# Kernel optimization log

Measured on AMD Instinct MI355X. Metric: run time of the kernel, lower is better.

The kernel has to match this reference:

```python
import jax, jax.numpy as jnp
import numpy as np

N_NODES = 100000


def _graph_conv(h, src, dst, W_rel, W_root, b):
    # PyG GraphConv with aggr='add':
    # out = lin_rel(scatter_add(h[src] -> dst)) + lin_root(h) + bias
    agg = jax.ops.segment_sum(h[src], dst, num_segments=N_NODES)  # [N, D]
    return agg @ W_rel.T + h @ W_root.T + b


def setup_inputs() -> dict:
    key = jax.random.key(0)
    ks = jax.random.split(key, 8)
    N, D, E = N_NODES, 128, 1600000
    s = 1.0 / np.sqrt(D)
    x = jax.random.normal(ks[0], (N, D), dtype=jnp.float32)
    edge_index = jax.random.randint(ks[1], (2, E), 0, N, dtype=jnp.int64)
    W1_rel = jax.random.normal(ks[2], (D, D), dtype=jnp.float32) * s
    W1_root = jax.random.normal(ks[3], (D, D), dtype=jnp.float32) * s
    b1 = jnp.zeros((D,), dtype=jnp.float32)
    W2_rel = jax.random.normal(ks[4], (D, D), dtype=jnp.float32) * s
    W2_root = jax.random.normal(ks[5], (D, D), dtype=jnp.float32) * s
    b2 = jnp.zeros((D,), dtype=jnp.float32)
    return {"x": x, "edge_index": edge_index, "W1_rel": W1_rel,
            "W1_root": W1_root, "b1": b1, "W2_rel": W2_rel,
            "W2_root": W2_root, "b2": b2}


def reference(x, edge_index, W1_rel, W1_root, b1, W2_rel, W2_root, b2):
    src, dst = edge_index[0], edge_index[1]
    h = _graph_conv(x, src, dst, W1_rel, W1_root, b1)
    h = jax.nn.relu(h)
    out = _graph_conv(h, src, dst, W2_rel, W2_root, b2)
    return out
```

## Files before the change

kernel.cpp:

```cpp
#include <hip/hip_runtime.h>

#define NN 100000
#define DIM 128
#define NE 1600000
#define NCHUNK 64
#define FILL_CHUNK (NE / NCHUNK)

typedef __attribute__((ext_vector_type(8))) short short8;
typedef __attribute__((ext_vector_type(4))) float f32x4;

__device__ __forceinline__ unsigned f2b(float f) {
    unsigned u = __float_as_uint(f);
    return (u + 0x7FFFu + ((u >> 16) & 1u)) >> 16;
}
__device__ __forceinline__ float blo(unsigned v) { return __uint_as_float(v << 16); }
__device__ __forceinline__ float bhi(unsigned v) { return __uint_as_float(v & 0xFFFF0000u); }

__device__ __forceinline__ long long didx(long long pos, int is64) {
    return is64 ? 2 * pos : pos;
}

__global__ void detect_kernel(const void* __restrict__ ei, int* __restrict__ flag) {
    __shared__ int any;
    if (threadIdx.x == 0) any = 0;
    __syncthreads();
    const int* p = (const int*)ei;
    int nz = 0;
    for (int i = threadIdx.x; i < 2048; i += 256) nz |= (p[2 * i + 1] != 0);
    if (nz) any = 1;
    __syncthreads();
    if (threadIdx.x == 0) flag[0] = any ? 0 : 1;
}

__global__ void cvt_kernel(const float* __restrict__ in, unsigned short* __restrict__ out, int n8) {
    int i = blockIdx.x * 256 + threadIdx.x;
    if (i >= n8) return;
    const float4* p = (const float4*)in + (size_t)i * 2;
    float4 a = p[0], b = p[1];
    uint4 o;
    o.x = f2b(a.x) | (f2b(a.y) << 16);
    o.y = f2b(a.z) | (f2b(a.w) << 16);
    o.z = f2b(b.x) | (f2b(b.y) << 16);
    o.w = f2b(b.z) | (f2b(b.w) << 16);
    ((uint4*)out)[i] = o;
}

__global__ void cvtw_kernel(const float* __restrict__ w0, const float* __restrict__ w1,
                            const float* __restrict__ w2, const float* __restrict__ w3,
                            unsigned short* __restrict__ o0, unsigned short* __restrict__ o1,
                            unsigned short* __restrict__ o2, unsigned short* __restrict__ o3) {
    int i = blockIdx.x * 256 + threadIdx.x;
    int which = i >> 11, j = i & 2047;
    const float* in = which == 0 ? w0 : which == 1 ? w1 : which == 2 ? w2 : w3;
    unsigned short* out = which == 0 ? o0 : which == 1 ? o1 : which == 2 ? o2 : o3;
    const float4* p = (const float4*)in + (size_t)j * 2;
    float4 a = p[0], b = p[1];
    uint4 o;
    o.x = f2b(a.x) | (f2b(a.y) << 16);
    o.y = f2b(a.z) | (f2b(a.w) << 16);
    o.z = f2b(b.x) | (f2b(b.y) << 16);
    o.w = f2b(b.z) | (f2b(b.w) << 16);
    ((uint4*)out)[j] = o;
}

__global__ void hist_kernel(const void* __restrict__ ei, int* __restrict__ deg,
                            const int* __restrict__ flag, int E) {
    int is64 = flag[0];
    const int* p = (const int*)ei;
    int base = blockIdx.x * 1024 + threadIdx.x;
    int d0 = -1, d1 = -1, d2 = -1, d3 = -1;
    if (base + 0 * 256 < E) d0 = p[didx((long long)E + base + 0 * 256, is64)];
    if (base + 1 * 256 < E) d1 = p[didx((long long)E + base + 1 * 256, is64)];
    if (base + 2 * 256 < E) d2 = p[didx((long long)E + base + 2 * 256, is64)];
    if (base + 3 * 256 < E) d3 = p[didx((long long)E + base + 3 * 256, is64)];
    if (d0 >= 0) atomicAdd(&deg[d0], 1);
    if (d1 >= 0) atomicAdd(&deg[d1], 1);
    if (d2 >= 0) atomicAdd(&deg[d2], 1);
    if (d3 >= 0) atomicAdd(&deg[d3], 1);
}

__global__ void scan1(const int* __restrict__ deg, int* __restrict__ offsets,
                      int* __restrict__ bsum, int n) {
    __shared__ int wsum[4];
    int t = threadIdx.x, lane = t & 63, w = t >> 6;
    int base = blockIdx.x * 1024 + t * 4;
    int a0 = base + 0 < n ? deg[base + 0] : 0;
    int a1 = base + 1 < n ? deg[base + 1] : 0;
    int a2 = base + 2 < n ? deg[base + 2] : 0;
    int a3 = base + 3 < n ? deg[base + 3] : 0;
    int s = a0 + a1 + a2 + a3;
    int x = s;
#pragma unroll
    for (int off = 1; off < 64; off <<= 1) {
        int y = __shfl_up(x, off, 64);
        if (lane >= off) x += y;
    }
    if (lane == 63) wsum[w] = x;
    __syncthreads();
    if (t == 0) {
        int c = 0;
#pragma unroll
        for (int k = 0; k < 4; k++) { int tmp = wsum[k]; wsum[k] = c; c += tmp; }
        bsum[blockIdx.x] = c;
    }
    __syncthreads();
    int excl = wsum[w] + (x - s);
    if (base + 0 < n) offsets[base + 0] = excl;
    if (base + 1 < n) offsets[base + 1] = excl + a0;
    if (base + 2 < n) offsets[base + 2] = excl + a0 + a1;
    if (base + 3 < n) offsets[base + 3] = excl + a0 + a1 + a2;
}

__global__ void scan2(int* __restrict__ bsum, int* __restrict__ offsets, int nb, int n) {
    __shared__ int w0tot;
    int t = threadIdx.x, lane = t & 63, w = t >> 6;
    int v = t < nb ? bsum[t] : 0;
    int x = v;
#pragma unroll
    for (int off = 1; off < 64; off <<= 1) {
        int y = __shfl_up(x, off, 64);
        if (lane >= off) x += y;
    }
    if (t == 63) w0tot = x;
    __syncthreads();
    int excl = x - v + (w ? w0tot : 0);
    if (t < nb) bsum[t] = excl;
    if (t == nb - 1) offsets[n] = excl + v;
}

__global__ void scan3(int* __restrict__ offsets, int* __restrict__ cursor,
                      const int* __restrict__ bsum, int n) {
    int base = blockIdx.x * 1024 + threadIdx.x * 4;
    int add = bsum[blockIdx.x];
#pragma unroll
    for (int j = 0; j < 4; j++) {
        int i = base + j;
        if (i < n) { int v = offsets[i] + add; offsets[i] = v; cursor[i] = v; }
    }
}

__global__ __launch_bounds__(256)
void fill_kernel(const void* __restrict__ ei, int* __restrict__ cursor,
                 int* __restrict__ csr_src, const int* __restrict__ flag,
                 int* __restrict__ claim, int E) {
    const int c = blockIdx.x >> 3;
    const int is64 = flag[0];
    const int* p = (const int*)ei;
    const int t = threadIdx.x;

    int xcd;
    asm volatile("s_getreg_b32 %0, hwreg(HW_REG_XCC_ID)" : "=s"(xcd));
    xcd &= 7;

    __shared__ int s_r;
    if (t == 0) {
        int got = -1;
#pragma unroll
        for (int k = 0; k < 8; k++) {
            int r = (xcd + k) & 7;
            if (atomicCAS(&claim[c * 8 + r], 0, 1) == 0) { got = r; break; }
        }
        s_r = got;
    }
    __syncthreads();
    const int r = s_r;
    if (r < 0) return;

    const int lo = r * (NN / 8), hi = lo + (NN / 8);
    const int beg = c * FILL_CHUNK;
    const int end = min(beg + FILL_CHUNK, E);
    for (int i = beg + t; i < end; i += 1024) {
        int e1 = i + 256, e2 = i + 512, e3 = i + 768;
        int d0 = p[didx((long long)E + i, is64)];
        int d1 = e1 < end ? p[didx((long long)E + e1, is64)] : -1;
        int d2 = e2 < end ? p[didx((long long)E + e2, is64)] : -1;
        int d3 = e3 < end ? p[didx((long long)E + e3, is64)] : -1;
        if (d0 >= lo && d0 < hi) csr_src[atomicAdd(&cursor[d0], 1)] = p[didx(i, is64)];
        if (d1 >= lo && d1 < hi) csr_src[atomicAdd(&cursor[d1], 1)] = p[didx(e1, is64)];
        if (d2 >= lo && d2 < hi) csr_src[atomicAdd(&cursor[d2], 1)] = p[didx(e2, is64)];
        if (d3 >= lo && d3 < hi) csr_src[atomicAdd(&cursor[d3], 1)] = p[didx(e3, is64)];
    }
}

__global__ void agg_kernel(const unsigned* __restrict__ hb,
                           const int* __restrict__ offsets,
                           const int* __restrict__ csr,
                           unsigned* __restrict__ aggb, int n) {
    int node = blockIdx.x * 4 + (threadIdx.x >> 6);
    int lane = threadIdx.x & 63;
    if (node >= n) return;
    int e = offsets[node], end = offsets[node + 1];
    float lo4[4] = {0.f, 0.f, 0.f, 0.f}, hi4[4] = {0.f, 0.f, 0.f, 0.f};
    for (; e + 8 <= end; e += 8) {
        int idx[8];
        unsigned vv[8];
#pragma unroll
        for (int j = 0; j < 8; j++) idx[j] = csr[e + j];
#pragma unroll
        for (int j = 0; j < 8; j++) vv[j] = hb[idx[j] * 64 + lane];
#pragma unroll
        for (int j = 0; j < 8; j++) { lo4[j & 3] += blo(vv[j]); hi4[j & 3] += bhi(vv[j]); }
    }
    for (; e + 4 <= end; e += 4) {
        int idx[4];
        unsigned vv[4];
#pragma unroll
        for (int j = 0; j < 4; j++) idx[j] = csr[e + j];
#pragma unroll
        for (int j = 0; j < 4; j++) vv[j] = hb[idx[j] * 64 + lane];
#pragma unroll
        for (int j = 0; j < 4; j++) { lo4[j] += blo(vv[j]); hi4[j] += bhi(vv[j]); }
    }
    for (; e < end; ++e) {
        unsigned v = hb[csr[e] * 64 + lane];
        lo4[0] += blo(v); hi4[0] += bhi(v);
    }
    float s0 = (lo4[0] + lo4[1]) + (lo4[2] + lo4[3]);
    float s1 = (hi4[0] + hi4[1]) + (hi4[2] + hi4[3]);
    aggb[node * 64 + lane] = f2b(s0) | (f2b(s1) << 16);
}

template <int OUTF32>
__global__ __launch_bounds__(256, 2)
void mfma_gemm(const unsigned short* __restrict__ A,
               const unsigned short* __restrict__ H,
               const unsigned short* __restrict__ Wr,
               const unsigned short* __restrict__ Wt,
               const float* __restrict__ bias,
               void* __restrict__ outp, int n) {
    __shared__ __align__(16) char sIn[128 * 256];
    __shared__ __align__(16) char sW[128 * 256];
    int t = threadIdx.x;
    int l = t & 63, w = t >> 6;
    int row0 = blockIdx.x * 128;
    int lr = l & 15;
    int lk = (l >> 4) << 3;

    f32x4 acc[2][8];
#pragma unroll
    for (int i = 0; i < 2; i++)
#pragma unroll
        for (int j = 0; j < 8; j++) acc[i][j] = (f32x4){0.f, 0.f, 0.f, 0.f};

    for (int phase = 0; phase < 2; ++phase) {
        const unsigned short* In = phase ? H : A;
        const unsigned short* W = phase ? Wt : Wr;
        __syncthreads();
#pragma unroll
        for (int q = 0; q < 8; q++) {
            int idx = q * 256 + t;
            int r = idx >> 4, c = idx & 15;
            int gr = row0 + r; if (gr > n - 1) gr = n - 1;
            uint4 v = ((const uint4*)In)[(size_t)gr * 16 + c];
            *(uint4*)(sIn + r * 256 + ((c * 16) ^ ((r & 7) << 4))) = v;
            uint4 wv = ((const uint4*)W)[r * 16 + c];
            *(uint4*)(sW + r * 256 + ((c * 16) ^ ((r & 7) << 4))) = wv;
        }
        __syncthreads();
#pragma unroll
        for (int ks = 0; ks < 4; ++ks) {
            int kb = (ks * 32 + lk) * 2;
            short8 av[2], bv[8];
#pragma unroll
            for (int mt = 0; mt < 2; mt++) {
                int r = w * 32 + mt * 16 + lr;
                av[mt] = *(const short8*)(sIn + r * 256 + (kb ^ ((r & 7) << 4)));
            }
#pragma unroll
            for (int nt = 0; nt < 8; nt++) {
                int cw = nt * 16 + lr;
                bv[nt] = *(const short8*)(sW + cw * 256 + (kb ^ ((cw & 7) << 4)));
            }
#pragma unroll
            for (int mt = 0; mt < 2; mt++)
#pragma unroll
                for (int nt = 0; nt < 8; nt++)
                    acc[mt][nt] = __builtin_amdgcn_mfma_f32_16x16x32_bf16(
                        av[mt], bv[nt], acc[mt][nt], 0, 0, 0);
        }
    }

    int rbase = row0 + w * 32 + ((l >> 4) << 2);
#pragma unroll
    for (int mt = 0; mt < 2; mt++) {
#pragma unroll
        for (int nt = 0; nt < 8; nt++) {
            int col = nt * 16 + lr;
            float bc = bias[col];
#pragma unroll
            for (int j = 0; j < 4; j++) {
                int row = rbase + mt * 16 + j;
                if (row < n) {
                    float v = acc[mt][nt][j] + bc;
                    if (OUTF32) {
                        ((float*)outp)[(size_t)row * DIM + col] = v;
                    } else {
                        v = fmaxf(v, 0.f);
                        ((unsigned short*)outp)[(size_t)row * DIM + col] =
                            (unsigned short)f2b(v);
                    }
                }
            }
        }
    }
}

extern "C" void kernel_launch(void* const* d_in, const int* in_sizes, int n_in,
                              void* d_out, int out_size, void* d_ws, size_t ws_size,
                              hipStream_t stream) {
    const int N = NN, E = NE;
    const float* x = (const float*)d_in[0];
    const void* ei = d_in[1];
    const float* W1r = (const float*)d_in[2];
    const float* W1t = (const float*)d_in[3];
    const float* b1 = (const float*)d_in[4];
    const float* W2r = (const float*)d_in[5];
    const float* W2t = (const float*)d_in[6];
    const float* b2 = (const float*)d_in[7];
    float* out = (float*)d_out;

    char* wsp = (char*)d_ws;
    auto alloc = [&](size_t bytes) {
        char* p = wsp;
        wsp += (bytes + 255) & ~(size_t)255;
        return p;
    };
    int* flag = (int*)alloc(4);
    int* deg = (int*)alloc((size_t)N * 4);
    int* claim = (int*)alloc((size_t)NCHUNK * 8 * 4);
    int* offsets = (int*)alloc((size_t)(N + 1) * 4);
    int* cursor = (int*)alloc((size_t)N * 4);
    int* bsum = (int*)alloc(512);
    int* csr_src = (int*)alloc((size_t)E * 4);
    unsigned short* w1rb = (unsigned short*)alloc(DIM * DIM * 2);
    unsigned short* w1tb = (unsigned short*)alloc(DIM * DIM * 2);
    unsigned short* w2rb = (unsigned short*)alloc(DIM * DIM * 2);
    unsigned short* w2tb = (unsigned short*)alloc(DIM * DIM * 2);
    unsigned short* xb = (unsigned short*)alloc((size_t)N * DIM * 2);
    unsigned short* aggb = (unsigned short*)alloc((size_t)N * DIM * 2);

    const int NB = (N + 1023) / 1024;

    hipMemsetAsync(deg, 0, (size_t)N * 4, stream);
    hipMemsetAsync(claim, 0, (size_t)NCHUNK * 8 * 4, stream);
    detect_kernel<<<1, 256, 0, stream>>>(ei, flag);

    cvt_kernel<<<(N * DIM / 8 + 255) / 256, 256, 0, stream>>>(x, xb, N * DIM / 8);
    cvtw_kernel<<<32, 256, 0, stream>>>(W1r, W1t, W2r, W2t, w1rb, w1tb, w2rb, w2tb);

    hist_kernel<<<(E + 1023) / 1024, 256, 0, stream>>>(ei, deg, flag, E);
    scan1<<<NB, 256, 0, stream>>>(deg, offsets, bsum, N);
    scan2<<<1, 128, 0, stream>>>(bsum, offsets, NB, N);
    scan3<<<NB, 256, 0, stream>>>(offsets, cursor, bsum, N);
    fill_kernel<<<NCHUNK * 8, 256, 0, stream>>>(ei, cursor, csr_src, flag, claim, E);

    agg_kernel<<<N / 4, 256, 0, stream>>>((const unsigned*)xb, offsets, csr_src,
                                          (unsigned*)aggb, N);
    mfma_gemm<0><<<(N + 127) / 128, 256, 0, stream>>>(aggb, xb, w1rb, w1tb, b1, xb, N);

    agg_kernel<<<N / 4, 256, 0, stream>>>((const unsigned*)xb, offsets, csr_src,
                                          (unsigned*)aggb, N);
    mfma_gemm<1><<<(N + 127) / 128, 256, 0, stream>>>(aggb, xb, w2rb, w2tb, b2, out, N);
}
```

Before: 455.0 us.

## Build CSR via two-level binned counting sort with shared-memory atomics

Replaces the global-atomic histogram, three-pass scan and XCD-partitioned atomic fill with a two-level bucket sort. Destinations are first binned into 128-node bins using per-block shared-memory histograms and scatter cursors, with packed (local dst, src) words staged in the aggregation buffer. A per-bin kernel then counts and places edges inside each bin to produce offsets and the CSR. The aim is to remove contended global atomics and scattered global writes during CSR construction. In exchange it adds a single-block scan over 64x782 counts and an extra pass over the edges.

```diff
diff --git a/kernel.cpp b/kernel.cpp
--- a/kernel.cpp
+++ b/kernel.cpp
@@ -3,8 +3,10 @@
 #define NN 100000
 #define DIM 128
 #define NE 1600000
-#define NCHUNK 64
-#define FILL_CHUNK (NE / NCHUNK)
+#define BINW 128
+#define NBIN 782
+#define NSB 64
+#define SCHUNK (NE / NSB)
 
 typedef __attribute__((ext_vector_type(8))) short short8;
 typedef __attribute__((ext_vector_type(4))) float f32x4;
@@ -63,33 +65,38 @@
     ((uint4*)out)[j] = o;
 }
 
-__global__ void hist_kernel(const void* __restrict__ ei, int* __restrict__ deg,
-                            const int* __restrict__ flag, int E) {
-    int is64 = flag[0];
+__global__ __launch_bounds__(512)
+void binhist_kernel(const void* __restrict__ ei, const int* __restrict__ flag,
+                    int* __restrict__ bcnt) {
+    __shared__ int h[NBIN];
+    for (int k = threadIdx.x; k < NBIN; k += 512) h[k] = 0;
+    __syncthreads();
+    const int is64 = flag[0];
     const int* p = (const int*)ei;
-    int base = blockIdx.x * 1024 + threadIdx.x;
-    int d0 = -1, d1 = -1, d2 = -1, d3 = -1;
-    if (base + 0 * 256 < E) d0 = p[didx((long long)E + base + 0 * 256, is64)];
-    if (base + 1 * 256 < E) d1 = p[didx((long long)E + base + 1 * 256, is64)];
-    if (base + 2 * 256 < E) d2 = p[didx((long long)E + base + 2 * 256, is64)];
-    if (base + 3 * 256 < E) d3 = p[didx((long long)E + base + 3 * 256, is64)];
-    if (d0 >= 0) atomicAdd(&deg[d0], 1);
-    if (d1 >= 0) atomicAdd(&deg[d1], 1);
-    if (d2 >= 0) atomicAdd(&deg[d2], 1);
-    if (d3 >= 0) atomicAdd(&deg[d3], 1);
-}
-
-__global__ void scan1(const int* __restrict__ deg, int* __restrict__ offsets,
-                      int* __restrict__ bsum, int n) {
-    __shared__ int wsum[4];
+    const int beg = blockIdx.x * SCHUNK, end = beg + SCHUNK;
+    for (int i = beg + (int)threadIdx.x; i < end; i += 512) {
+        unsigned b = ((unsigned)p[didx((long long)NE + i, is64)]) >> 7;
+        if (b < NBIN) atomicAdd(&h[b], 1);
+    }
+    __syncthreads();
+    for (int k = threadIdx.x; k < NBIN; k += 512)
+        bcnt[blockIdx.x * NBIN + k] = h[k];
+}
+
+__global__ __launch_bounds__(1024)
+void binscan_kernel(const int* __restrict__ bcnt, int* __restrict__ start,
+                    int* __restrict__ binofs) {
+    __shared__ int tot[NBIN];
+    __shared__ int wsum[16];
     int t = threadIdx.x, lane = t & 63, w = t >> 6;
-    int base = blockIdx.x * 1024 + t * 4;
-    int a0 = base + 0 < n ? deg[base + 0] : 0;
-    int a1 = base + 1 < n ? deg[base + 1] : 0;
-    int a2 = base + 2 < n ? deg[base + 2] : 0;
-    int a3 = base + 3 < n ? deg[base + 3] : 0;
-    int s = a0 + a1 + a2 + a3;
-    int x = s;
+    for (int k = t; k < NBIN; k += 1024) {
+        int s = 0;
+        for (int b = 0; b < NSB; b++) s += bcnt[b * NBIN + k];
+        tot[k] = s;
+    }
+    __syncthreads();
+    int v = (t < NBIN) ? tot[t] : 0;
+    int x = v;
 #pragma unroll
     for (int off = 1; off < 64; off <<= 1) {
         int y = __shfl_up(x, off, 64);
@@ -97,88 +104,92 @@
     }
     if (lane == 63) wsum[w] = x;
     __syncthreads();
-    if (t == 0) {
-        int c = 0;
-#pragma unroll
-        for (int k = 0; k < 4; k++) { int tmp = wsum[k]; wsum[k] = c; c += tmp; }
-        bsum[blockIdx.x] = c;
-    }
-    __syncthreads();
-    int excl = wsum[w] + (x - s);
-    if (base + 0 < n) offsets[base + 0] = excl;
-    if (base + 1 < n) offsets[base + 1] = excl + a0;
-    if (base + 2 < n) offsets[base + 2] = excl + a0 + a1;
-    if (base + 3 < n) offsets[base + 3] = excl + a0 + a1 + a2;
-}
-
-__global__ void scan2(int* __restrict__ bsum, int* __restrict__ offsets, int nb, int n) {
-    __shared__ int w0tot;
-    int t = threadIdx.x, lane = t & 63, w = t >> 6;
-    int v = t < nb ? bsum[t] : 0;
-    int x = v;
-#pragma unroll
-    for (int off = 1; off < 64; off <<= 1) {
-        int y = __shfl_up(x, off, 64);
-        if (lane >= off) x += y;
-    }
-    if (t == 63) w0tot = x;
-    __syncthreads();
-    int excl = x - v + (w ? w0tot : 0);
-    if (t < nb) bsum[t] = excl;
-    if (t == nb - 1) offsets[n] = excl + v;
-}
-
-__global__ void scan3(int* __restrict__ offsets, int* __restrict__ cursor,
-                      const int* __restrict__ bsum, int n) {
-    int base = blockIdx.x * 1024 + threadIdx.x * 4;
-    int add = bsum[blockIdx.x];
-#pragma unroll
-    for (int j = 0; j < 4; j++) {
-        int i = base + j;
-        if (i < n) { int v = offsets[i] + add; offsets[i] = v; cursor[i] = v; }
-    }
-}
-
-__global__ __launch_bounds__(256)
-void fill_kernel(const void* __restrict__ ei, int* __restrict__ cursor,
-                 int* __restrict__ csr_src, const int* __restrict__ flag,
-                 int* __restrict__ claim, int E) {
-    const int c = blockIdx.x >> 3;
+    if (w == 0) {
+        int s = (lane < 16) ? wsum[lane] : 0;
+#pragma unroll
+        for (int off = 1; off < 16; off <<= 1) {
+            int y = __shfl_up(s, off, 64);
+            if (lane >= off) s += y;
+        }
+        if (lane < 16) wsum[lane] = s;
+    }
+    __syncthreads();
+    int excl = (w ? wsum[w - 1] : 0) + (x - v);
+    if (t < NBIN) binofs[t] = excl;
+    if (t == NBIN - 1) binofs[NBIN] = excl + v;
+    __syncthreads();
+    for (int k = t; k < NBIN; k += 1024) {
+        int acc = binofs[k];
+        for (int b = 0; b < NSB; b++) {
+            start[b * NBIN + k] = acc;
+            acc += bcnt[b * NBIN + k];
+        }
+    }
+}
+
+__global__ __launch_bounds__(512)
+void binscatter_kernel(const void* __restrict__ ei, const int* __restrict__ flag,
+                       const int* __restrict__ start, unsigned* __restrict__ ebin) {
+    __shared__ int cur[NBIN];
+    for (int k = threadIdx.x; k < NBIN; k += 512)
+        cur[k] = start[blockIdx.x * NBIN + k];
+    __syncthreads();
     const int is64 = flag[0];
     const int* p = (const int*)ei;
-    const int t = threadIdx.x;
-
-    int xcd;
-    asm volatile("s_getreg_b32 %0, hwreg(HW_REG_XCC_ID)" : "=s"(xcd));
-    xcd &= 7;
-
-    __shared__ int s_r;
+    const int beg = blockIdx.x * SCHUNK, end = beg + SCHUNK;
+    for (int i = beg + (int)threadIdx.x; i < end; i += 2048) {
+        int dd[4], ss[4];
+#pragma unroll
+        for (int j = 0; j < 4; j++) {
+            int e = i + j * 512;
+            if (e < end) {
+                dd[j] = p[didx((long long)NE + e, is64)];
+                ss[j] = p[didx(e, is64)];
+            } else { dd[j] = -1; ss[j] = 0; }
+        }
+#pragma unroll
+        for (int j = 0; j < 4; j++) {
+            unsigned b = ((unsigned)dd[j]) >> 7;
+            if (dd[j] >= 0 && b < NBIN) {
+                int pos = atomicAdd(&cur[b], 1);
+                if ((unsigned)pos < (unsigned)NE)
+                    ebin[pos] = ((unsigned)(dd[j] & 127) << 17) | (unsigned)ss[j];
+            }
+        }
+    }
+}
+
+__global__ __launch_bounds__(256)
+void binfin_kernel(const unsigned* __restrict__ ebin, const int* __restrict__ binofs,
+                   int* __restrict__ offsets, int* __restrict__ csr) {
+    __shared__ int cnt[BINW];
+    __shared__ int excl[BINW];
+    int t = threadIdx.x;
+    if (t < BINW) cnt[t] = 0;
+    __syncthreads();
+    int k = blockIdx.x;
+    int beg = binofs[k];
+    int end = binofs[k + 1];
+    if (beg < 0) beg = 0;
+    if (end > NE) end = NE;
+    for (int i = beg + t; i < end; i += 256) atomicAdd(&cnt[ebin[i] >> 17], 1);
+    __syncthreads();
     if (t == 0) {
-        int got = -1;
-#pragma unroll
-        for (int k = 0; k < 8; k++) {
-            int r = (xcd + k) & 7;
-            if (atomicCAS(&claim[c * 8 + r], 0, 1) == 0) { got = r; break; }
-        }
-        s_r = got;
-    }
-    __syncthreads();
-    const int r = s_r;
-    if (r < 0) return;
-
-    const int lo = r * (NN / 8), hi = lo + (NN / 8);
-    const int beg = c * FILL_CHUNK;
-    const int end = min(beg + FILL_CHUNK, E);
-    for (int i = beg + t; i < end; i += 1024) {
-        int e1 = i + 256, e2 = i + 512, e3 = i + 768;
-        int d0 = p[didx((long long)E + i, is64)];
-        int d1 = e1 < end ? p[didx((long long)E + e1, is64)] : -1;
-        int d2 = e2 < end ? p[didx((long long)E + e2, is64)] : -1;
-        int d3 = e3 < end ? p[didx((long long)E + e3, is64)] : -1;
-        if (d0 >= lo && d0 < hi) csr_src[atomicAdd(&cursor[d0], 1)] = p[didx(i, is64)];
-        if (d1 >= lo && d1 < hi) csr_src[atomicAdd(&cursor[d1], 1)] = p[didx(e1, is64)];
-        if (d2 >= lo && d2 < hi) csr_src[atomicAdd(&cursor[d2], 1)] = p[didx(e2, is64)];
-        if (d3 >= lo && d3 < hi) csr_src[atomicAdd(&cursor[d3], 1)] = p[didx(e3, is64)];
+        int a = 0;
+        for (int r = 0; r < BINW; r++) { excl[r] = a; a += cnt[r]; }
+    }
+    __syncthreads();
+    if (t < BINW) {
+        int node = k * BINW + t;
+        if (node < NN) offsets[node] = beg + excl[t];
+        cnt[t] = excl[t];
+    }
+    if (k == 0 && t == 0) offsets[NN] = NE;
+    __syncthreads();
+    for (int i = beg + t; i < end; i += 256) {
+        unsigned c = ebin[i];
+        int pos = atomicAdd(&cnt[c >> 17], 1);
+        if (beg + pos < NE) csr[beg + pos] = (int)(c & 0x1FFFF);
     }
 }
 
@@ -308,7 +319,7 @@
 extern "C" void kernel_launch(void* const* d_in, const int* in_sizes, int n_in,
                               void* d_out, int out_size, void* d_ws, size_t ws_size,
                               hipStream_t stream) {
-    const int N = NN, E = NE;
+    const int N = NN;
     const float* x = (const float*)d_in[0];
     const void* ei = d_in[1];
     const float* W1r = (const float*)d_in[2];
@@ -326,39 +337,34 @@
         return p;
     };
     int* flag = (int*)alloc(4);
-    int* deg = (int*)alloc((size_t)N * 4);
-    int* claim = (int*)alloc((size_t)NCHUNK * 8 * 4);
+    int* bcnt = (int*)alloc((size_t)NSB * NBIN * 4);
+    int* start = (int*)alloc((size_t)NSB * NBIN * 4);
+    int* binofs = (int*)alloc((size_t)(NBIN + 1) * 4);
     int* offsets = (int*)alloc((size_t)(N + 1) * 4);
-    int* cursor = (int*)alloc((size_t)N * 4);
-    int* bsum = (int*)alloc(512);
-    int* csr_src = (int*)alloc((size_t)E * 4);
+    int* csr = (int*)alloc((size_t)NE * 4);
     unsigned short* w1rb = (unsigned short*)alloc(DIM * DIM * 2);
     unsigned short* w1tb = (unsigned short*)alloc(DIM * DIM * 2);
     unsigned short* w2rb = (unsigned short*)alloc(DIM * DIM * 2);
     unsigned short* w2tb = (unsigned short*)alloc(DIM * DIM * 2);
     unsigned short* xb = (unsigned short*)alloc((size_t)N * DIM * 2);
     unsigned short* aggb = (unsigned short*)alloc((size_t)N * DIM * 2);
-
-    const int NB = (N + 1023) / 1024;
-
-    hipMemsetAsync(deg, 0, (size_t)N * 4, stream);
-    hipMemsetAsync(claim, 0, (size_t)NCHUNK * 8 * 4, stream);
+    unsigned* ebin = (unsigned*)aggb;
+
     detect_kernel<<<1, 256, 0, stream>>>(ei, flag);
 
     cvt_kernel<<<(N * DIM / 8 + 255) / 256, 256, 0, stream>>>(x, xb, N * DIM / 8);
     cvtw_kernel<<<32, 256, 0, stream>>>(W1r, W1t, W2r, W2t, w1rb, w1tb, w2rb, w2tb);
 
-    hist_kernel<<<(E + 1023) / 1024, 256, 0, stream>>>(ei, deg, flag, E);
-    scan1<<<NB, 256, 0, stream>>>(deg, offsets, bsum, N);
-    scan2<<<1, 128, 0, stream>>>(bsum, offsets, NB, N);
-    scan3<<<NB, 256, 0, stream>>>(offsets, cursor, bsum, N);
-    fill_kernel<<<NCHUNK * 8, 256, 0, stream>>>(ei, cursor, csr_src, flag, claim, E);
-
-    agg_kernel<<<N / 4, 256, 0, stream>>>((const unsigned*)xb, offsets, csr_src,
+    binhist_kernel<<<NSB, 512, 0, stream>>>(ei, flag, bcnt);
+    binscan_kernel<<<1, 1024, 0, stream>>>(bcnt, start, binofs);
+    binscatter_kernel<<<NSB, 512, 0, stream>>>(ei, flag, start, ebin);
+    binfin_kernel<<<NBIN, 256, 0, stream>>>(ebin, binofs, offsets, csr);
+
+    agg_kernel<<<N / 4, 256, 0, stream>>>((const unsigned*)xb, offsets, csr,
                                           (unsigned*)aggb, N);
     mfma_gemm<0><<<(N + 127) / 128, 256, 0, stream>>>(aggb, xb, w1rb, w1tb, b1, xb, N);
 
-    agg_kernel<<<N / 4, 256, 0, stream>>>((const unsigned*)xb, offsets, csr_src,
+    agg_kernel<<<N / 4, 256, 0, stream>>>((const unsigned*)xb, offsets, csr,
                                           (unsigned*)aggb, N);
     mfma_gemm<1><<<(N + 127) / 128, 256, 0, stream>>>(aggb, xb, w2rb, w2tb, b2, out, N);
 }
```

Measured after the change: 366.2 us. 1.24x faster.
